# Kernel tuning notes

Hardware: AMD Instinct MI355X
Metric: run time of the kernel (lower is better)

Reference implementation:

```python
import jax, jax.numpy as jnp
import numpy as np

PSP_SIZES = (1, 3, 6, 8)  # KV length S = 1 + 9 + 36 + 64 = 110
BN_EPS = 1e-5


def conv1x1(x, W, b):
    # x: [B,C,H,W], W: [O,C], b: [O] -> [B,O,H,W]
    return jnp.einsum('bchw,oc->bohw', x, W) + b[None, :, None, None]


def psp(f):
    # f: [B,C,H,W] -> [B,C,S]; H,W divisible by all sizes so adaptive pool == block mean
    B, C, H, W = f.shape
    priors = []
    for s in PSP_SIZES:
        p = f.reshape(B, C, s, H // s, s, W // s).mean(axis=(3, 5))  # [B,C,s,s]
        priors.append(p.reshape(B, C, s * s))
    return jnp.concatenate(priors, axis=-1)  # [B,C,S]


def setup_inputs() -> dict:
    key = jax.random.key(0)
    ks = jax.random.split(key, 8)
    B, C, H, W = 8, 512, 72, 72
    Kc, Vc = 256, 256
    return {
        'x': jax.random.normal(ks[0], (B, C, H, W), jnp.float32),
        'Wk': jax.random.normal(ks[1], (Kc, C), jnp.float32) * (1.0 / np.sqrt(C)),
        'bk': jax.random.normal(ks[2], (Kc,), jnp.float32) * 0.01,
        'gamma': jnp.ones((Kc,), jnp.float32),
        'beta': jnp.zeros((Kc,), jnp.float32),
        'rmean': jnp.zeros((Kc,), jnp.float32),
        'rvar': jax.random.uniform(ks[3], (Kc,), jnp.float32, 0.5, 1.5),
        'Wv': jax.random.normal(ks[4], (Vc, C), jnp.float32) * (1.0 / np.sqrt(C)),
        'bv': jax.random.normal(ks[5], (Vc,), jnp.float32) * 0.01,
        'Ww': jax.random.normal(ks[6], (C, Vc), jnp.float32) * (1.0 / np.sqrt(Vc)),
        'bw': jnp.zeros((C,), jnp.float32),
    }


def reference(x, Wk, bk, gamma, beta, rmean, rvar, Wv, bv, Ww, bw):
    B, C, H, W = x.shape
    Kc = Wk.shape[0]
    Vc = Wv.shape[0]
    # f_value: conv1x1, then PSP -> value [B,S,Vc]
    value = psp(conv1x1(x, Wv, bv)).transpose(0, 2, 1)
    # f_key == f_query: conv1x1 + BN(inference) + ReLU
    k = conv1x1(x, Wk, bk)
    inv = gamma / jnp.sqrt(rvar + BN_EPS)
    k = jax.nn.relu(k * inv[None, :, None, None] + (beta - rmean * inv)[None, :, None, None])
    query = k.reshape(B, Kc, H * W).transpose(0, 2, 1)  # [B,HW,Kc]
    keyt = psp(k)  # [B,Kc,S]
    sim = jnp.einsum('bnk,bks->bns', query, keyt) * (Kc ** -0.5)
    sim = jax.nn.softmax(sim, axis=-1)
    context = jnp.einsum('bns,bsv->bnv', sim, value)  # [B,HW,Vc]
    context = context.transpose(0, 2, 1).reshape(B, Vc, H, W)
    return conv1x1(context, Ww, bw)
```

## Files before the change

### kernel.cpp

```cpp
#include <hip/hip_runtime.h>
#include <hip/hip_bf16.h>

#define HW    5184
#define WIDTH 72
#define CIN   512
#define KC    256
#define VC    256
#define NS    110
#define NSP   112
#define SPV   128
#define BATCH 8

typedef unsigned short u16;
typedef unsigned int   u32;
typedef __attribute__((ext_vector_type(8))) short bf16x8;
typedef __attribute__((ext_vector_type(4))) float f32x4;

typedef const __attribute__((address_space(1))) u32* gp_t;
typedef __attribute__((address_space(3))) u32* lp_t;

__device__ __forceinline__ u32 f2bf1(float f) {
    u32 u = __float_as_uint(f);
    return (u + 0x7FFFu + ((u >> 16) & 1u)) >> 16;
}
__device__ __forceinline__ u32 pack2(float a, float b) {
    return f2bf1(a) | (f2bf1(b) << 16);
}
__device__ __forceinline__ float bf2f(u16 h) {
    return __uint_as_float((u32)h << 16);
}

__global__ void prep_kernel(const float* __restrict__ bk, const float* __restrict__ gamma,
                            const float* __restrict__ beta, const float* __restrict__ rmean,
                            const float* __restrict__ rvar, float* __restrict__ inv_out,
                            float* __restrict__ bc_out) {
    int i = threadIdx.x;
    float inv = gamma[i] * rsqrtf(rvar[i] + 1e-5f);
    inv_out[i] = inv;
    bc_out[i]  = bk[i] * inv + beta[i] - rmean[i] * inv;
}

__global__ __launch_bounds__(256) void cvt_w_kernel(
    const float* __restrict__ Wk, const float* __restrict__ Ww, const float* __restrict__ Wv,
    u16* __restrict__ Wkbf, u16* __restrict__ Wwbf, u16* __restrict__ Wvbf)
{
    int j = (blockIdx.x * 256 + threadIdx.x) * 4;
    const float* s; u16* d;
    if (j < KC * CIN)          { s = Wk; d = Wkbf; }
    else if (j < 2 * KC * CIN) { j -= KC * CIN;     s = Ww; d = Wwbf; }
    else                       { j -= 2 * KC * CIN; s = Wv; d = Wvbf; }
    float4 v = *(const float4*)&s[j];
    uint2 u;
    u.x = pack2(v.x, v.y);
    u.y = pack2(v.z, v.w);
    *(uint2*)&d[j] = u;
}

__global__ __launch_bounds__(256) void transpose_cvt_kernel(
    const float* __restrict__ in, u16* __restrict__ out, int C)
{
    const int z  = blockIdx.z;
    const int n0 = blockIdx.x * 64;
    const int k0 = blockIdx.y * 64;
    __shared__ float t[64][65];
    const int tx = threadIdx.x & 63, ty = threadIdx.x >> 6;
    const float* src = in + ((size_t)z * C + k0) * HW + n0;
#pragma unroll
    for (int i = 0; i < 16; i++)
        t[ty + i * 4][tx] = src[(size_t)(ty + i * 4) * HW + tx];
    __syncthreads();
    u16* dst = out + ((size_t)z * HW + n0) * C + k0;
    const int kp  = (threadIdx.x & 31) * 2;
    const int nl0 = threadIdx.x >> 5;
#pragma unroll
    for (int j = 0; j < 8; j++) {
        int nl = nl0 + j * 8;
        u32 u = pack2(t[kp][nl], t[kp + 1][nl]);
        *(u32*)&dst[(size_t)nl * C + kp] = u;
    }
}

__global__ __launch_bounds__(256) void gemm_nt_bf16(
    const u16* __restrict__ A, const u16* __restrict__ B, float* __restrict__ C,
    u16* __restrict__ Ct,
    int M, int N, int K, int nbx, int nby,
    const float* __restrict__ scale, const float* __restrict__ bias, int relu)
{
    const int tot = nbx * nby * BATCH;
    const int q = tot >> 3, r = tot & 7;
    const int xcd = blockIdx.x & 7;
    const int wg  = (xcd < r ? xcd * (q + 1) : r * (q + 1) + (xcd - r) * q) + (blockIdx.x >> 3);
    const int mb_ = wg % nby;
    const int nb_ = (wg / nby) % nbx;
    const int z   = wg / (nby * nbx);

    const int n0 = nb_ * 128;
    const int m0 = mb_ * 128;
    const size_t boff = (size_t)z * N * K;
    const size_t coff = (size_t)z * M * N;
    const int tid  = threadIdx.x;
    const int wid  = tid >> 6;
    const int lane = tid & 63;

    __shared__ __align__(16) u16 As[3][4][128][8];
    __shared__ __align__(16) u16 Bs[3][4][128][8];

    const int kg0  = (wid & 1) * 2;
    const int half = (wid >> 1) * 64;

    const u16* gA = A + (size_t)(m0 + half + lane) * K + kg0 * 8;
    int nIdx = n0 + half + lane;
    if (nIdx > N - 1) nIdx = N - 1;
    const u16* gB = B + boff + (size_t)nIdx * K + kg0 * 8;

    const int wm  = (wid >> 1) * 64;
    const int wn  = (wid & 1) * 64;
    const int l16 = lane & 15;
    const int lq  = lane >> 4;

    f32x4 acc[4][4];
#pragma unroll
    for (int mi = 0; mi < 4; mi++)
#pragma unroll
        for (int ni = 0; ni < 4; ni++)
            acc[mi][ni] = (f32x4){0.f, 0.f, 0.f, 0.f};

#define STAGE(d, kk)                                                                              \
    __builtin_amdgcn_global_load_lds((gp_t)(gA + (kk)),     (lp_t)&As[d][kg0][half][0], 16, 0, 0);\
    __builtin_amdgcn_global_load_lds((gp_t)(gA + (kk) + 8), (lp_t)&As[d][kg0+1][half][0],16, 0, 0);\
    __builtin_amdgcn_global_load_lds((gp_t)(gB + (kk)),     (lp_t)&Bs[d][kg0][half][0], 16, 0, 0);\
    __builtin_amdgcn_global_load_lds((gp_t)(gB + (kk) + 8), (lp_t)&Bs[d][kg0+1][half][0],16, 0, 0);

    const int NT = K >> 5;
    STAGE(0, 0)
    STAGE(1, 32)

    int cur = 0;
    for (int t = 0; t < NT; ++t) {
        if (t + 1 < NT) { asm volatile("s_waitcnt vmcnt(4)" ::: "memory"); }
        else            { asm volatile("s_waitcnt vmcnt(0)" ::: "memory"); }
        __builtin_amdgcn_s_barrier();
        __builtin_amdgcn_sched_barrier(0);

        if (t + 2 < NT) {
            int nb = cur + 2; if (nb >= 3) nb -= 3;
            STAGE(nb, (t + 2) * 32)
        }

        bf16x8 af[4], bf[4];
#pragma unroll
        for (int i = 0; i < 4; i++) {
            af[i] = *(const bf16x8*)&As[cur][lq][wm + i * 16 + l16][0];
            bf[i] = *(const bf16x8*)&Bs[cur][lq][wn + i * 16 + l16][0];
        }
        __builtin_amdgcn_s_setprio(1);
#pragma unroll
        for (int mi = 0; mi < 4; mi++)
#pragma unroll
            for (int ni = 0; ni < 4; ni++)
                acc[mi][ni] = __builtin_amdgcn_mfma_f32_16x16x32_bf16(
                    af[mi], bf[ni], acc[mi][ni], 0, 0, 0);
        __builtin_amdgcn_s_setprio(0);

        cur = (cur == 2) ? 0 : cur + 1;
    }
#undef STAGE

#pragma unroll
    for (int mi = 0; mi < 4; mi++) {
        const int mb = m0 + wm + mi * 16 + lq * 4;
        float sc[4], bi[4];
#pragma unroll
        for (int r2 = 0; r2 < 4; r2++) {
            sc[r2] = scale ? scale[mb + r2] : 1.0f;
            bi[r2] = bias  ? bias[mb + r2]  : 0.0f;
        }
#pragma unroll
        for (int ni = 0; ni < 4; ni++) {
            const int n = n0 + wn + ni * 16 + l16;
            if (n < N) {
                float v[4];
#pragma unroll
                for (int r2 = 0; r2 < 4; r2++) {
                    v[r2] = acc[mi][ni][r2] * sc[r2] + bi[r2];
                    if (relu) v[r2] = fmaxf(v[r2], 0.f);
                }
                if (C) {
#pragma unroll
                    for (int r2 = 0; r2 < 4; r2++)
                        C[coff + (size_t)(mb + r2) * N + n] = v[r2];
                }
                if (Ct) {
                    uint2 u;
                    u.x = pack2(v[0], v[1]);
                    u.y = pack2(v[2], v[3]);
                    *(uint2*)&Ct[(size_t)z * N * M + (size_t)n * M + mb] = u;
                }
            }
        }
    }
}

__global__ __launch_bounds__(256) void rowpool_k_kernel(
    const u16* __restrict__ kT, float* __restrict__ rp)
{
    const int y = blockIdx.x;
    const int b = blockIdx.y;
    const int c = threadIdx.x;
    const u16* src = kT + ((size_t)b * HW + (size_t)y * WIDTH) * KC + c;
    float s9[8]  = {0.f, 0.f, 0.f, 0.f, 0.f, 0.f, 0.f, 0.f};
    float s12[6] = {0.f, 0.f, 0.f, 0.f, 0.f, 0.f};
#pragma unroll
    for (int x = 0; x < 72; x++) {
        float v = bf2f(src[(size_t)x * KC]);
        s9[x / 9] += v;
        s12[x / 12] += v;
    }
    float* dst = rp + (((size_t)b * 72 + y) * 15) * KC + c;
    float tot = 0.f;
#pragma unroll
    for (int g = 0; g < 8; g++) dst[(size_t)g * KC] = s9[g];
#pragma unroll
    for (int g = 0; g < 6; g++) { dst[(size_t)(8 + g) * KC] = s12[g]; tot += s12[g]; }
    dst[(size_t)14 * KC] = tot;
}

__global__ __launch_bounds__(256) void binpool_k_kernel(
    const float* __restrict__ rp, u16* __restrict__ keytb)
{
    const int s = blockIdx.x;
    const int b = blockIdx.y;
    const int c = threadIdx.x;
    char* ob = (char*)keytb + (size_t)b * NSP * KC * 2;
    float sum = 0.f, scl = 0.f;
    const float* rpb = rp + (size_t)b * 72 * 15 * KC + c;
    if (s < NS) {
        if (s == 0) {
#pragma unroll 8
            for (int y = 0; y < 72; y++) sum += rpb[((size_t)y * 15 + 14) * KC];
            scl = 1.f / 5184.f;
        } else if (s < 10) {
            const int t = s - 1, gy = t / 3, gx = t - gy * 3;
#pragma unroll 8
            for (int i = 0; i < 24; i++) {
                const int y = gy * 24 + i;
                sum += rpb[((size_t)y * 15 + 8 + 2 * gx) * KC]
                     + rpb[((size_t)y * 15 + 9 + 2 * gx) * KC];
            }
            scl = 1.f / 576.f;
        } else if (s < 46) {
            const int t = s - 10, gy = t / 6, gx = t - gy * 6;
#pragma unroll
            for (int i = 0; i < 12; i++) {
                const int y = gy * 12 + i;
                sum += rpb[((size_t)y * 15 + 8 + gx) * KC];
            }
            scl = 1.f / 144.f;
        } else {
            const int t = s - 46, gy = t >> 3, gx = t & 7;
#pragma unroll
            for (int i = 0; i < 9; i++) {
                const int y = gy * 9 + i;
                sum += rpb[((size_t)y * 15 + gx) * KC];
            }
            scl = 1.f / 81.f;
        }
    }
    const int byte = s * 512 + ((c * 2) ^ ((s & 7) << 4));
    *(u16*)(ob + byte) = (s < NS) ? (u16)f2bf1(sum * scl) : (u16)0;
}

__global__ __launch_bounds__(256) void value_mfma_kernel(
    const u16* __restrict__ A, const u16* __restrict__ Bp,
    const float* __restrict__ bv, u16* __restrict__ valT)
{
    const int m0 = blockIdx.x * 128;
    const int b  = blockIdx.y;
    const int tid  = threadIdx.x;
    const int wid  = tid >> 6;
    const int lane = tid & 63;

    __shared__ __align__(16) u16 As[4][128][8];
    __shared__ __align__(16) u16 Bs[4][128][8];

    const int kg0  = (wid & 1) * 2;
    const int half = (wid >> 1) * 64;

    const u16* gA = A + (size_t)(m0 + half + lane) * CIN + kg0 * 8;
    const u16* gB = Bp + (size_t)b * SPV * CIN + (size_t)(half + lane) * CIN + kg0 * 8;

    lp_t lA0 = (lp_t)&As[kg0][half][0];
    lp_t lA1 = (lp_t)&As[kg0 + 1][half][0];
    lp_t lB0 = (lp_t)&Bs[kg0][half][0];
    lp_t lB1 = (lp_t)&Bs[kg0 + 1][half][0];

    const int wm  = (wid >> 1) * 64;
    const int wn  = (wid & 1) * 64;
    const int l16 = lane & 15;
    const int lq  = lane >> 4;

    f32x4 acc[4][4];
#pragma unroll
    for (int mi = 0; mi < 4; mi++)
#pragma unroll
        for (int ni = 0; ni < 4; ni++)
            acc[mi][ni] = (f32x4){0.f, 0.f, 0.f, 0.f};

    for (int k0 = 0; k0 < CIN; k0 += 32) {
        __builtin_amdgcn_global_load_lds((gp_t)(gA + k0),     lA0, 16, 0, 0);
        __builtin_amdgcn_global_load_lds((gp_t)(gA + k0 + 8), lA1, 16, 0, 0);
        __builtin_amdgcn_global_load_lds((gp_t)(gB + k0),     lB0, 16, 0, 0);
        __builtin_amdgcn_global_load_lds((gp_t)(gB + k0 + 8), lB1, 16, 0, 0);
        __syncthreads();

        bf16x8 af[4], bf[4];
#pragma unroll
        for (int i = 0; i < 4; i++) {
            af[i] = *(const bf16x8*)&As[lq][wm + i * 16 + l16][0];
            bf[i] = *(const bf16x8*)&Bs[lq][wn + i * 16 + l16][0];
        }
#pragma unroll
        for (int mi = 0; mi < 4; mi++)
#pragma unroll
            for (int ni = 0; ni < 4; ni++)
                acc[mi][ni] = __builtin_amdgcn_mfma_f32_16x16x32_bf16(
                    af[mi], bf[ni], acc[mi][ni], 0, 0, 0);
        __syncthreads();
    }

    char* vb = (char*)valT + (size_t)b * VC * SPV * 2;
#pragma unroll
    for (int mi = 0; mi < 4; mi++) {
        const int mb = m0 + wm + mi * 16 + lq * 4;
        float bi[4];
#pragma unroll
        for (int r = 0; r < 4; r++) bi[r] = bv[mb + r];
#pragma unroll
        for (int ni = 0; ni < 4; ni++) {
            const int n = wn + ni * 16 + l16;
#pragma unroll
            for (int r = 0; r < 4; r++) {
                const int v = mb + r;
                const int byte = v * 256 + ((n * 2) ^ ((v & 7) << 4));
                *(u16*)(vb + byte) = (u16)f2bf1(acc[mi][ni][r] + bi[r]);
            }
        }
    }
}

__global__ __launch_bounds__(128) void psp_pool_px_kernel(
    const float* __restrict__ in, u16* __restrict__ out)
{
    const int c = blockIdx.x;
    const int b = blockIdx.y;
    const int t = threadIdx.x;
    __shared__ float4 row4[1296];
    __shared__ float aux[100];
    float* row = (float*)row4;
    const float* src = in + ((size_t)b * CIN + c) * HW;
    for (int idx = t; idx < 1296; idx += 128)
        row4[idx] = *(const float4*)(src + idx * 4);
    __syncthreads();
    if (t < 64) {
        int r0 = (t >> 3) * 9, c0 = (t & 7) * 9;
        float s = 0.f;
        for (int i = 0; i < 9; i++)
            for (int j = 0; j < 9; j++) s += row[(r0 + i) * WIDTH + c0 + j];
        aux[t] = s;
    } else if (t < 100) {
        int tt = t - 64;
        int r0 = (tt / 6) * 12, c0 = (tt % 6) * 12;
        float s = 0.f;
        for (int i = 0; i < 12; i++)
            for (int j = 0; j < 12; j++) s += row[(r0 + i) * WIDTH + c0 + j];
        aux[64 + tt] = s;
    }
    __syncthreads();
    u16* ob = out + (size_t)b * SPV * CIN + c;
    if (t < 64) ob[(size_t)(46 + t) * CIN] = (u16)f2bf1(aux[t] * (1.f / 81.f));
    if (t < 36) ob[(size_t)(10 + t) * CIN] = (u16)f2bf1(aux[64 + t] * (1.f / 144.f));
    if (t < 9) {
        int r = t / 3, cc = t % 3;
        float s4 = aux[64 + (2 * r) * 6 + 2 * cc] + aux[64 + (2 * r) * 6 + 2 * cc + 1]
                 + aux[64 + (2 * r + 1) * 6 + 2 * cc] + aux[64 + (2 * r + 1) * 6 + 2 * cc + 1];
        ob[(size_t)(1 + t) * CIN] = (u16)f2bf1(s4 * (1.f / 576.f));
    }
    if (t == 0) {
        float s = 0.f;
        for (int i = 0; i < 64; i++) s += aux[i];
        ob[0] = (u16)f2bf1(s * (1.f / 5184.f));
    }
    if (t < 18) ob[(size_t)(110 + t) * CIN] = 0;
}

__global__ __launch_bounds__(256, 3) void attn_mfma_kernel(
    const u16* __restrict__ qT, const u16* __restrict__ keyt,
    const u16* __restrict__ valT, const u16* __restrict__ Wwb,
    const float* __restrict__ bw, float* __restrict__ out)
{
    const int b    = blockIdx.y;
    const int tid  = threadIdx.x;
    const int wid  = tid >> 6;
    const int lane = tid & 63;
    const int l16  = lane & 15;
    const int lq   = lane >> 4;
    const int nblk = blockIdx.x * 64;
    const int px0  = nblk + wid * 16;

    __shared__ __align__(16) u16 SM[24576];
    char* base = (char*)SM;
    const int POFF = 32768;

    const char* gk = (const char*)keyt + (size_t)b * (NSP * KC * 2);
    const char* gv = (const char*)valT + (size_t)b * (VC * SPV * 2);

#pragma unroll
    for (int i = 0; i < 8; i++) {
        const int o = (wid * 8 + i) * 1024;
        __builtin_amdgcn_global_load_lds((gp_t)(gk + o + lane * 16), (lp_t)(base + o), 16, 0, 0);
    }

    const u16* qrow = qT + ((size_t)b * HW + px0 + l16) * KC + lq * 8;
    bf16x8 aq[8];
#pragma unroll
    for (int ks = 0; ks < 8; ks++) aq[ks] = *(const bf16x8*)(qrow + ks * 32);

    __syncthreads();

    f32x4 acc[7];
#pragma unroll
    for (int ni = 0; ni < 7; ni++) acc[ni] = (f32x4){0.f, 0.f, 0.f, 0.f};
#pragma unroll
    for (int ks = 0; ks < 8; ks++) {
#pragma unroll
        for (int ni = 0; ni < 4; ni++) {
            const int s = ni * 16 + l16;
            const int byte = s * 512 + ((ks * 64 + lq * 16) ^ ((s & 7) << 4));
            bf16x8 bk = *(const bf16x8*)(base + byte);
            acc[ni] = __builtin_amdgcn_mfma_f32_16x16x32_bf16(aq[ks], bk, acc[ni], 0, 0, 0);
        }
    }
    __syncthreads();

#pragma unroll
    for (int i = 0; i < 6; i++) {
        const int o = (wid * 6 + i) * 1024;
        __builtin_amdgcn_global_load_lds((gp_t)(gk + 32768 + o + lane * 16), (lp_t)(base + o), 16, 0, 0);
    }
    __syncthreads();

#pragma unroll
    for (int ks = 0; ks < 8; ks++) {
#pragma unroll
        for (int ni = 4; ni < 7; ni++) {
            const int s = ni * 16 + l16;
            const int srow = s - 64;
            const int byte = srow * 512 + ((ks * 64 + lq * 16) ^ ((srow & 7) << 4));
            bf16x8 bk = *(const bf16x8*)(base + byte);
            acc[ni] = __builtin_amdgcn_mfma_f32_16x16x32_bf16(aq[ks], bk, acc[ni], 0, 0, 0);
        }
    }
    if (l16 >= 14) acc[6] = (f32x4){-1e30f, -1e30f, -1e30f, -1e30f};
    __syncthreads();

#pragma unroll
    for (int i = 0; i < 8; i++) {
        const int o = (wid * 8 + i) * 1024;
        __builtin_amdgcn_global_load_lds((gp_t)(gv + o + lane * 16), (lp_t)(base + o), 16, 0, 0);
    }

    float mx[4], sm[4], rn[4];
#pragma unroll
    for (int r = 0; r < 4; r++) {
        float m = acc[0][r];
#pragma unroll
        for (int ni = 1; ni < 7; ni++) m = fmaxf(m, acc[ni][r]);
        m = fmaxf(m, __shfl_xor(m, 1));
        m = fmaxf(m, __shfl_xor(m, 2));
        m = fmaxf(m, __shfl_xor(m, 4));
        m = fmaxf(m, __shfl_xor(m, 8));
        mx[r] = m * 0.0625f;
        sm[r] = 0.f;
    }

    const int prow = wid * 16 + 4 * lq;
#pragma unroll
    for (int ni = 0; ni < 7; ni++) {
#pragma unroll
        for (int r = 0; r < 4; r++) {
            float p = __expf(acc[ni][r] * 0.0625f - mx[r]);
            sm[r] += p;
            const int row = prow + r;
            const int byte = POFF + row * 256 + (((ni * 16 + l16) * 2) ^ ((row & 7) << 4));
            *(u16*)(base + byte) = (u16)f2bf1(p);
        }
    }
    if (l16 < 2) {
#pragma unroll
        for (int r = 0; r < 4; r++) {
            const int row = prow + r;
            const int byte = POFF + row * 256 + ((224 + l16 * 16) ^ ((row & 7) << 4));
            *(bf16x8*)(base + byte) = (bf16x8){0, 0, 0, 0, 0, 0, 0, 0};
        }
    }
#pragma unroll
    for (int r = 0; r < 4; r++) {
        float s = sm[r];
        s += __shfl_xor(s, 1);
        s += __shfl_xor(s, 2);
        s += __shfl_xor(s, 4);
        s += __shfl_xor(s, 8);
        rn[r] = 1.f / s;
    }
    __syncthreads();

    f32x4 acc2[16];
#pragma unroll
    for (int ni = 0; ni < 16; ni++) acc2[ni] = (f32x4){0.f, 0.f, 0.f, 0.f};
    const int arow = wid * 16 + l16;
    const int aswz = (arow & 7) << 4;
#pragma unroll
    for (int ks = 0; ks < 4; ks++) {
        const int pbyte = POFF + arow * 256 + ((ks * 64 + lq * 16) ^ aswz);
        bf16x8 pa = *(const bf16x8*)(base + pbyte);
#pragma unroll
        for (int ni = 0; ni < 8; ni++) {
            const int v = ni * 16 + l16;
            const int vbyte = v * 256 + ((ks * 64 + lq * 16) ^ ((v & 7) << 4));
            bf16x8 bvv = *(const bf16x8*)(base + vbyte);
            acc2[ni] = __builtin_amdgcn_mfma_f32_16x16x32_bf16(pa, bvv, acc2[ni], 0, 0, 0);
        }
    }
    __syncthreads();

#pragma unroll
    for (int i = 0; i < 8; i++) {
        const int o = (wid * 8 + i) * 1024;
        __builtin_amdgcn_global_load_lds((gp_t)(gv + 32768 + o + lane * 16), (lp_t)(base + o), 16, 0, 0);
    }
    __syncthreads();

#pragma unroll
    for (int ks = 0; ks < 4; ks++) {
        const int pbyte = POFF + arow * 256 + ((ks * 64 + lq * 16) ^ aswz);
        bf16x8 pa = *(const bf16x8*)(base + pbyte);
#pragma unroll
        for (int ni = 8; ni < 16; ni++) {
            const int vrow = (ni - 8) * 16 + l16;
            const int vbyte = vrow * 256 + ((ks * 64 + lq * 16) ^ ((vrow & 7) << 4));
            bf16x8 bvv = *(const bf16x8*)(base + vbyte);
            acc2[ni] = __builtin_amdgcn_mfma_f32_16x16x32_bf16(pa, bvv, acc2[ni], 0, 0, 0);
        }
    }
    __syncthreads();

#pragma unroll
    for (int ni = 0; ni < 16; ni++) {
#pragma unroll
        for (int r = 0; r < 4; r++) {
            const int row = prow + r;
            const int v = ni * 16 + l16;
            const int byte = row * 512 + ((v * 2) ^ ((row & 7) << 4));
            *(u16*)(base + byte) = (u16)f2bf1(acc2[ni][r] * rn[r]);
        }
    }
    __syncthreads();

    const int wc0 = wid * 128;
    float* outb = out + (size_t)b * CIN * HW + nblk;
    char* scr = base + POFF + wid * 4096;

#pragma unroll
    for (int ch = 0; ch < 2; ch++) {
        f32x4 accg[4][4];
#pragma unroll
        for (int pi = 0; pi < 4; pi++)
#pragma unroll
            for (int cj = 0; cj < 4; cj++)
                accg[pi][cj] = (f32x4){0.f, 0.f, 0.f, 0.f};

        const u16* wwbase = Wwb + (size_t)(wc0 + ch * 64 + l16) * VC + lq * 8;
#pragma unroll
        for (int ks = 0; ks < 8; ks++) {
            bf16x8 af[4];
#pragma unroll
            for (int pi = 0; pi < 4; pi++) {
                const int px = pi * 16 + l16;
                const int byte = px * 512 + ((ks * 64 + lq * 16) ^ ((px & 7) << 4));
                af[pi] = *(const bf16x8*)(base + byte);
            }
            bf16x8 bfr[4];
#pragma unroll
            for (int cj = 0; cj < 4; cj++)
                bfr[cj] = *(const bf16x8*)(wwbase + (size_t)cj * 16 * VC + ks * 32);
#pragma unroll
            for (int pi = 0; pi < 4; pi++)
#pragma unroll
                for (int cj = 0; cj < 4; cj++)
                    accg[pi][cj] = __builtin_amdgcn_mfma_f32_16x16x32_bf16(
                        af[pi], bfr[cj], accg[pi][cj], 0, 0, 0);
        }

#pragma unroll
        for (int cj = 0; cj < 4; cj++) {
            const int cl = l16;
            const int swz = (cl & 7) << 5;
#pragma unroll
            for (int pi = 0; pi < 4; pi++)
#pragma unroll
                for (int r = 0; r < 4; r++) {
                    const int px = pi * 16 + 4 * lq + r;
                    *(float*)(scr + cl * 256 + ((px * 4) ^ swz)) = accg[pi][cj][r];
                }
#pragma unroll
            for (int cr = 0; cr < 4; cr++) {
                const int cl2 = cr * 4 + lq;
                const int swz2 = (cl2 & 7) << 5;
                float4 vv = *(const float4*)(scr + cl2 * 256 + ((l16 * 16) ^ swz2));
                const int c = wc0 + ch * 64 + cj * 16 + cl2;
                const float bb = bw[c];
                vv.x += bb; vv.y += bb; vv.z += bb; vv.w += bb;
                *(float4*)&outb[(size_t)c * HW + l16 * 4] = vv;
            }
        }
    }
}

extern "C" void kernel_launch(void* const* d_in, const int* in_sizes, int n_in,
                              void* d_out, int out_size, void* d_ws, size_t ws_size,
                              hipStream_t stream)
{
    const float* x     = (const float*)d_in[0];
    const float* Wk    = (const float*)d_in[1];
    const float* bk    = (const float*)d_in[2];
    const float* gamma = (const float*)d_in[3];
    const float* beta  = (const float*)d_in[4];
    const float* rmean = (const float*)d_in[5];
    const float* rvar  = (const float*)d_in[6];
    const float* Wv    = (const float*)d_in[7];
    const float* bv    = (const float*)d_in[8];
    const float* Ww    = (const float*)d_in[9];
    const float* bw    = (const float*)d_in[10];
    float* out = (float*)d_out;

    float* ws    = (float*)d_ws;
    float* rp    = ws;
    u16*   xT    = (u16*)(rp + (size_t)BATCH * 72 * 15 * KC);
    u16*   kT    = xT + (size_t)BATCH * HW * CIN;
    u16*   pxb   = kT + (size_t)BATCH * HW * KC;
    u16*   keytb = pxb + (size_t)BATCH * SPV * CIN;
    u16*   valT  = keytb + (size_t)BATCH * NSP * KC;
    u16*   Wkbf  = valT + (size_t)BATCH * VC * SPV;
    u16*   Wwbf  = Wkbf + (size_t)KC * CIN;
    u16*   Wvbf  = Wwbf + (size_t)CIN * VC;
    float* inv   = (float*)(Wvbf + (size_t)KC * CIN);
    float* bc    = inv + 256;

    prep_kernel<<<1, 256, 0, stream>>>(bk, gamma, beta, rmean, rvar, inv, bc);
    cvt_w_kernel<<<384, 256, 0, stream>>>(Wk, Ww, Wv, Wkbf, Wwbf, Wvbf);
    psp_pool_px_kernel<<<dim3(CIN, BATCH), 128, 0, stream>>>(x, pxb);
    transpose_cvt_kernel<<<dim3(HW / 64, CIN / 64, BATCH), 256, 0, stream>>>(x, xT, CIN);
    {
        const int nbx = (HW + 127) / 128, nby = KC / 128;
        gemm_nt_bf16<<<nbx * nby * BATCH, 256, 0, stream>>>(
            Wkbf, xT, nullptr, kT, KC, HW, CIN, nbx, nby, inv, bc, 1);
    }
    rowpool_k_kernel<<<dim3(72, BATCH), 256, 0, stream>>>(kT, rp);
    binpool_k_kernel<<<dim3(NSP, BATCH), 256, 0, stream>>>(rp, keytb);
    value_mfma_kernel<<<dim3(2, BATCH), 256, 0, stream>>>(Wvbf, pxb, bv, valT);
    attn_mfma_kernel<<<dim3(HW / 64, BATCH), 256, 0, stream>>>(
        kT, keytb, valT, Wwbf, bw, out);
}
```

Before: 158.2 us.

## Fuse x transpose-convert with row pooling, add separate bin-pool pass for PSP

The separate PSP pooling kernel that re-read all of x is removed. The transpose/bf16-convert kernel now tiles by image row and also writes per-row partial sums over 9- and 12-wide column bins into a new fp32 workspace. A small bin-pool kernel then combines these row partials into the pooled bf16 prior tensor. This drops one full pass over the 85 MB input at the cost of an extra launch, extra workspace traffic, and a different transpose tile shape (72 pixels by 64 channels with float4 loads).

Result: no change. 160.6 us (+1.5%).

```diff
diff --git a/kernel.cpp b/kernel.cpp
--- a/kernel.cpp
+++ b/kernel.cpp
@@ -56,27 +56,98 @@
     *(uint2*)&d[j] = u;
 }
 
-__global__ __launch_bounds__(256) void transpose_cvt_kernel(
-    const float* __restrict__ in, u16* __restrict__ out, int C)
-{
-    const int z  = blockIdx.z;
-    const int n0 = blockIdx.x * 64;
-    const int k0 = blockIdx.y * 64;
-    __shared__ float t[64][65];
-    const int tx = threadIdx.x & 63, ty = threadIdx.x >> 6;
-    const float* src = in + ((size_t)z * C + k0) * HW + n0;
-#pragma unroll
-    for (int i = 0; i < 16; i++)
-        t[ty + i * 4][tx] = src[(size_t)(ty + i * 4) * HW + tx];
-    __syncthreads();
-    u16* dst = out + ((size_t)z * HW + n0) * C + k0;
-    const int kp  = (threadIdx.x & 31) * 2;
-    const int nl0 = threadIdx.x >> 5;
-#pragma unroll
-    for (int j = 0; j < 8; j++) {
-        int nl = nl0 + j * 8;
-        u32 u = pack2(t[kp][nl], t[kp + 1][nl]);
-        *(u32*)&dst[(size_t)nl * C + kp] = u;
+__global__ __launch_bounds__(256) void transpose_pool_kernel(
+    const float* __restrict__ in, u16* __restrict__ xT, float* __restrict__ rpx)
+{
+    const int y  = blockIdx.x;
+    const int c0 = blockIdx.y * 64;
+    const int b  = blockIdx.z;
+    const int t  = threadIdx.x;
+    __shared__ float tile[64][73];
+    const float* src = in + ((size_t)b * CIN + c0) * HW + (size_t)y * WIDTH;
+    for (int idx = t; idx < 64 * 18; idx += 256) {
+        const int cc = idx / 18, seg = idx - cc * 18;
+        float4 v = *(const float4*)(src + (size_t)cc * HW + seg * 4);
+        tile[cc][seg * 4 + 0] = v.x;
+        tile[cc][seg * 4 + 1] = v.y;
+        tile[cc][seg * 4 + 2] = v.z;
+        tile[cc][seg * 4 + 3] = v.w;
+    }
+    __syncthreads();
+    {
+        const int kp  = (t & 31) * 2;
+        const int nl0 = t >> 5;
+        u16* dst = xT + ((size_t)b * HW + (size_t)y * WIDTH) * CIN + c0 + kp;
+#pragma unroll
+        for (int j = 0; j < 9; j++) {
+            const int px = nl0 + j * 8;
+            u32 u = pack2(tile[kp][px], tile[kp + 1][px]);
+            *(u32*)&dst[(size_t)px * CIN] = u;
+        }
+    }
+    if (t < 64) {
+        float s9[8]  = {0.f, 0.f, 0.f, 0.f, 0.f, 0.f, 0.f, 0.f};
+        float s12[6] = {0.f, 0.f, 0.f, 0.f, 0.f, 0.f};
+#pragma unroll
+        for (int x = 0; x < 72; x++) {
+            float v = tile[t][x];
+            s9[x / 9] += v;
+            s12[x / 12] += v;
+        }
+        float* dst = rpx + (((size_t)b * 72 + y) * 15) * CIN + c0 + t;
+        float tot = 0.f;
+#pragma unroll
+        for (int g = 0; g < 8; g++) dst[(size_t)g * CIN] = s9[g];
+#pragma unroll
+        for (int g = 0; g < 6; g++) { dst[(size_t)(8 + g) * CIN] = s12[g]; tot += s12[g]; }
+        dst[(size_t)14 * CIN] = tot;
+    }
+}
+
+__global__ __launch_bounds__(256) void binpool_px_kernel(
+    const float* __restrict__ rpx, u16* __restrict__ pxb)
+{
+    const int s = blockIdx.x;
+    const int b = blockIdx.y;
+    const int t = threadIdx.x;
+    u16* ob = pxb + ((size_t)b * SPV + s) * CIN;
+    if (s >= NS) { ob[t] = 0; ob[t + 256] = 0; return; }
+#pragma unroll
+    for (int h = 0; h < 2; h++) {
+        const int c = t + h * 256;
+        const float* rpb = rpx + (size_t)b * 72 * 15 * CIN + c;
+        float sum = 0.f, scl = 0.f;
+        if (s == 0) {
+#pragma unroll 8
+            for (int y = 0; y < 72; y++) sum += rpb[((size_t)y * 15 + 14) * CIN];
+            scl = 1.f / 5184.f;
+        } else if (s < 10) {
+            const int tt = s - 1, gy = tt / 3, gx = tt - gy * 3;
+#pragma unroll 8
+            for (int i = 0; i < 24; i++) {
+                const int y = gy * 24 + i;
+                sum += rpb[((size_t)y * 15 + 8 + 2 * gx) * CIN]
+                     + rpb[((size_t)y * 15 + 9 + 2 * gx) * CIN];
+            }
+            scl = 1.f / 576.f;
+        } else if (s < 46) {
+            const int tt = s - 10, gy = tt / 6, gx = tt - gy * 6;
+#pragma unroll
+            for (int i = 0; i < 12; i++) {
+                const int y = gy * 12 + i;
+                sum += rpb[((size_t)y * 15 + 8 + gx) * CIN];
+            }
+            scl = 1.f / 144.f;
+        } else {
+            const int tt = s - 46, gy = tt >> 3, gx = tt & 7;
+#pragma unroll
+            for (int i = 0; i < 9; i++) {
+                const int y = gy * 9 + i;
+                sum += rpb[((size_t)y * 15 + gx) * CIN];
+            }
+            scl = 1.f / 81.f;
+        }
+        ob[c] = (u16)f2bf1(sum * scl);
     }
 }
 
@@ -348,51 +419,6 @@
     }
 }
 
-__global__ __launch_bounds__(128) void psp_pool_px_kernel(
-    const float* __restrict__ in, u16* __restrict__ out)
-{
-    const int c = blockIdx.x;
-    const int b = blockIdx.y;
-    const int t = threadIdx.x;
-    __shared__ float4 row4[1296];
-    __shared__ float aux[100];
-    float* row = (float*)row4;
-    const float* src = in + ((size_t)b * CIN + c) * HW;
-    for (int idx = t; idx < 1296; idx += 128)
-        row4[idx] = *(const float4*)(src + idx * 4);
-    __syncthreads();
-    if (t < 64) {
-        int r0 = (t >> 3) * 9, c0 = (t & 7) * 9;
-        float s = 0.f;
-        for (int i = 0; i < 9; i++)
-            for (int j = 0; j < 9; j++) s += row[(r0 + i) * WIDTH + c0 + j];
-        aux[t] = s;
-    } else if (t < 100) {
-        int tt = t - 64;
-        int r0 = (tt / 6) * 12, c0 = (tt % 6) * 12;
-        float s = 0.f;
-        for (int i = 0; i < 12; i++)
-            for (int j = 0; j < 12; j++) s += row[(r0 + i) * WIDTH + c0 + j];
-        aux[64 + tt] = s;
-    }
-    __syncthreads();
-    u16* ob = out + (size_t)b * SPV * CIN + c;
-    if (t < 64) ob[(size_t)(46 + t) * CIN] = (u16)f2bf1(aux[t] * (1.f / 81.f));
-    if (t < 36) ob[(size_t)(10 + t) * CIN] = (u16)f2bf1(aux[64 + t] * (1.f / 144.f));
-    if (t < 9) {
-        int r = t / 3, cc = t % 3;
-        float s4 = aux[64 + (2 * r) * 6 + 2 * cc] + aux[64 + (2 * r) * 6 + 2 * cc + 1]
-                 + aux[64 + (2 * r + 1) * 6 + 2 * cc] + aux[64 + (2 * r + 1) * 6 + 2 * cc + 1];
-        ob[(size_t)(1 + t) * CIN] = (u16)f2bf1(s4 * (1.f / 576.f));
-    }
-    if (t == 0) {
-        float s = 0.f;
-        for (int i = 0; i < 64; i++) s += aux[i];
-        ob[0] = (u16)f2bf1(s * (1.f / 5184.f));
-    }
-    if (t < 18) ob[(size_t)(110 + t) * CIN] = 0;
-}
-
 __global__ __launch_bounds__(256, 3) void attn_mfma_kernel(
     const u16* __restrict__ qT, const u16* __restrict__ keyt,
     const u16* __restrict__ valT, const u16* __restrict__ Wwb,
@@ -644,8 +670,9 @@
     float* out = (float*)d_out;
 
     float* ws    = (float*)d_ws;
-    float* rp    = ws;
-    u16*   xT    = (u16*)(rp + (size_t)BATCH * 72 * 15 * KC);
+    float* rpk   = ws;
+    float* rpx   = rpk + (size_t)BATCH * 72 * 15 * KC;
+    u16*   xT    = (u16*)(rpx + (size_t)BATCH * 72 * 15 * CIN);
     u16*   kT    = xT + (size_t)BATCH * HW * CIN;
     u16*   pxb   = kT + (size_t)BATCH * HW * KC;
     u16*   keytb = pxb + (size_t)BATCH * SPV * CIN;
@@ -658,15 +685,15 @@
 
     prep_kernel<<<1, 256, 0, stream>>>(bk, gamma, beta, rmean, rvar, inv, bc);
     cvt_w_kernel<<<384, 256, 0, stream>>>(Wk, Ww, Wv, Wkbf, Wwbf, Wvbf);
-    psp_pool_px_kernel<<<dim3(CIN, BATCH), 128, 0, stream>>>(x, pxb);
-    transpose_cvt_kernel<<<dim3(HW / 64, CIN / 64, BATCH), 256, 0, stream>>>(x, xT, CIN);
+    transpose_pool_kernel<<<dim3(72, CIN / 64, BATCH), 256, 0, stream>>>(x, xT, rpx);
+    binpool_px_kernel<<<dim3(SPV, BATCH), 256, 0, stream>>>(rpx, pxb);
     {
         const int nbx = (HW + 127) / 128, nby = KC / 128;
         gemm_nt_bf16<<<nbx * nby * BATCH, 256, 0, stream>>>(
             Wkbf, xT, nullptr, kT, KC, HW, CIN, nbx, nby, inv, bc, 1);
     }
-    rowpool_k_kernel<<<dim3(72, BATCH), 256, 0, stream>>>(kT, rp);
-    binpool_k_kernel<<<dim3(NSP, BATCH), 256, 0, stream>>>(rp, keytb);
+    rowpool_k_kernel<<<dim3(72, BATCH), 256, 0, stream>>>(kT, rpk);
+    binpool_k_kernel<<<dim3(NSP, BATCH), 256, 0, stream>>>(rpk, keytb);
     value_mfma_kernel<<<dim3(2, BATCH), 256, 0, stream>>>(Wvbf, pxb, bv, valT);
     attn_mfma_kernel<<<dim3(HW / 64, BATCH), 256, 0, stream>>>(
         kT, keytb, valT, Wwbf, bw, out);
```
